# Kernel tuning notes

Hardware: AMD Instinct MI355X
Metric: run time of the kernel (lower is better)

## Reference

```python
import jax, jax.numpy as jnp
import numpy as np

B, T, C, H = 8, 2048, 1024, 64


def build_rope_cache(seq_len, dim):
    half = dim // 2
    inv_freq = 1.0 / (10000.0 ** (jnp.arange(half, dtype=jnp.float32) / half))
    t = jnp.arange(seq_len, dtype=jnp.float32)
    freqs = t[:, None] * inv_freq[None, :]          # (T, half)
    cos = jnp.repeat(jnp.cos(freqs), 2, axis=-1)    # (T, dim) interleaved
    sin = jnp.repeat(jnp.sin(freqs), 2, axis=-1)
    return cos, sin


def apply_rope(x, cos, sin):
    # x: (B, T, H); cos/sin: (T, H)
    x1 = x[..., ::2]
    x2 = x[..., 1::2]
    rot = jnp.stack([-x2, x1], axis=-1).reshape(x.shape)
    return x * cos[None] + rot * sin[None]


def setup_inputs() -> dict:
    key = jax.random.key(0)
    kx, kq, kk, kv = jax.random.split(key, 4)
    scale = 1.0 / np.sqrt(C)
    return {
        "x": jax.random.normal(kx, (B, T, C), dtype=jnp.float32),
        "Wq": jax.random.normal(kq, (C, H), dtype=jnp.float32) * scale,
        "Wk": jax.random.normal(kk, (C, H), dtype=jnp.float32) * scale,
        "Wv": jax.random.normal(kv, (C, H), dtype=jnp.float32) * scale,
    }


def reference(x, Wq, Wk, Wv):
    Bc, Tc, _ = x.shape
    head_size = Wq.shape[1]
    cos, sin = build_rope_cache(Tc, head_size)

    q = apply_rope(x @ Wq, cos, sin)   # (B, T, H)
    k = apply_rope(x @ Wk, cos, sin)   # (B, T, H)
    v = x @ Wv                          # (B, T, H)

    # full TxT masked softmax attention (matches original non-fused path)
    wei = jnp.einsum('bth,bsh->bts', q, k) * (head_size ** -0.5)  # (B, T, T)
    causal = jnp.tril(jnp.ones((Tc, Tc), dtype=bool))
    wei = jnp.where(causal[None], wei, -jnp.inf)
    wei = jax.nn.softmax(wei, axis=-1)
    # dropout p=0 (eval mode) -> identity
    return jnp.einsum('bts,bsh->bth', wei, v)
```

## Files before the change

kernel.cpp:

```cpp
#include <hip/hip_runtime.h>
#include <cmath>

#define Tn  2048
#define Cn  1024
#define Hn  64
#define BTn 16384

typedef _Float16 f16x8 __attribute__((ext_vector_type(8)));
typedef _Float16 f16x4 __attribute__((ext_vector_type(4)));
typedef _Float16 f16x2 __attribute__((ext_vector_type(2)));
typedef float    f32x4 __attribute__((ext_vector_type(4)));

__global__ __launch_bounds__(256) void prep_w_kernel(
    const float* __restrict__ Wq, const float* __restrict__ Wk,
    const float* __restrict__ Wv, _Float16* __restrict__ Wt)
{
    __shared__ float ts[64][65];
    const int blk = blockIdx.x;
    const int p   = blk >> 4;
    const int c0  = (blk & 15) * 64;
    const float* __restrict__ W = (p == 0) ? Wq : (p == 1) ? Wk : Wv;
    const int tid = threadIdx.x;
    #pragma unroll
    for (int it = 0; it < 16; it++) {
        int idx = tid + it * 256;
        int c = idx >> 6, n = idx & 63;
        ts[c][n] = W[(size_t)(c0 + c) * Hn + n];
    }
    __syncthreads();
    #pragma unroll
    for (int it = 0; it < 16; it++) {
        int idx = tid + it * 256;
        int n = idx >> 6, c = idx & 63;
        Wt[(size_t)(p * 64 + n) * Cn + c0 + c] = (_Float16)ts[c][n];
    }
}

#define XSP 1032

__global__ __launch_bounds__(256) void proj_kernel(
    const float* __restrict__ x, const _Float16* __restrict__ Wt,
    _Float16* __restrict__ qh, _Float16* __restrict__ kh, _Float16* __restrict__ vT)
{
    __shared__ _Float16 xs[32 * XSP];
    const int row0 = blockIdx.x * 32;
    const int tid  = threadIdx.x;
    const int wave = tid >> 6, lane = tid & 63;
    const int quad = lane >> 4, l15 = lane & 15;

    #pragma unroll 8
    for (int it = 0; it < 32; it++) {
        int idx = tid + it * 256;
        int r = idx >> 8, c4 = idx & 255;
        float4 xv = *(const float4*)&x[(size_t)(row0 + r) * Cn + c4 * 4];
        f16x4 hv = { (_Float16)xv.x, (_Float16)xv.y, (_Float16)xv.z, (_Float16)xv.w };
        *(f16x4*)&xs[r * XSP + c4 * 4] = hv;
    }
    __syncthreads();

    f32x4 acc[2][3] = {};
    const _Float16* __restrict__ wb = Wt + (size_t)(wave * 48 + l15) * Cn + quad * 8;

    #pragma unroll 4
    for (int kc = 0; kc < Cn; kc += 32) {
        f16x8 b0 = *(const f16x8*)&wb[kc];
        f16x8 b1 = *(const f16x8*)&wb[16 * Cn + kc];
        f16x8 b2 = *(const f16x8*)&wb[32 * Cn + kc];
        f16x8 a0 = *(const f16x8*)&xs[(     l15) * XSP + kc + quad * 8];
        f16x8 a1 = *(const f16x8*)&xs[(16 + l15) * XSP + kc + quad * 8];
        acc[0][0] = __builtin_amdgcn_mfma_f32_16x16x32_f16(a0, b0, acc[0][0], 0, 0, 0);
        acc[1][0] = __builtin_amdgcn_mfma_f32_16x16x32_f16(a1, b0, acc[1][0], 0, 0, 0);
        acc[0][1] = __builtin_amdgcn_mfma_f32_16x16x32_f16(a0, b1, acc[0][1], 0, 0, 0);
        acc[1][1] = __builtin_amdgcn_mfma_f32_16x16x32_f16(a1, b1, acc[1][1], 0, 0, 0);
        acc[0][2] = __builtin_amdgcn_mfma_f32_16x16x32_f16(a0, b2, acc[0][2], 0, 0, 0);
        acc[1][2] = __builtin_amdgcn_mfma_f32_16x16x32_f16(a1, b2, acc[1][2], 0, 0, 0);
    }

    const int bidx = row0 >> 11;
    #pragma unroll
    for (int nt = 0; nt < 3; nt++) {
        const int n = wave * 48 + nt * 16 + l15;
        const int p = n >> 6;
        const int h = n & 63;
        if (p < 2) {
            _Float16* __restrict__ outb = (p == 0) ? qh : kh;
            const float invf = __expf(-0.2878231366242557f * (float)(h >> 1));
            #pragma unroll
            for (int mt = 0; mt < 2; mt++) {
                #pragma unroll
                for (int r = 0; r < 4; r++) {
                    int   row = row0 + mt * 16 + quad * 4 + r;
                    float val = acc[mt][nt][r];
                    float partner = __shfl_xor(val, 1, 64);
                    float ang = (float)(row & (Tn - 1)) * invf;
                    float sv, cv;
                    __sincosf(ang, &sv, &cv);
                    float res = (h & 1) ? fmaf(val, cv,  partner * sv)
                                        : fmaf(val, cv, -partner * sv);
                    if (p == 0) res *= 0.125f;
                    float resn = __shfl_xor(res, 1, 64);
                    if (!(l15 & 1)) {
                        f16x2 pk = { (_Float16)res, (_Float16)resn };
                        *(f16x2*)&outb[(size_t)row * Hn + h] = pk;
                    }
                }
            }
        } else {
            #pragma unroll
            for (int mt = 0; mt < 2; mt++) {
                int t = (row0 & (Tn - 1)) + mt * 16 + quad * 4;
                f16x4 pv = { (_Float16)acc[mt][nt][0], (_Float16)acc[mt][nt][1],
                             (_Float16)acc[mt][nt][2], (_Float16)acc[mt][nt][3] };
                *(f16x4*)&vT[((size_t)bidx * Hn + h) * Tn + t] = pv;
            }
        }
    }
}

#define PSP 72

__global__ __launch_bounds__(128) void attn_kernel(
    const _Float16* __restrict__ qh, const _Float16* __restrict__ kh,
    const _Float16* __restrict__ vT, float* __restrict__ out)
{
    __shared__ _Float16 ps[2][16 * PSP];
    __shared__ float ocomb[2][16][65];
    __shared__ float mlcomb[2][2][16];

    const int blk = blockIdx.x;
    const int b   = blk & 7;
    const int j   = blk >> 3;
    const int jm  = j & 31, g = j >> 5;
    const int qt  = (g == 0) ? (127 - jm)
                  : (g == 1) ? (64 + jm)
                  : (g == 2) ? (63 - jm) : jm;
    const int t0  = qt * 16;
    const int tid = threadIdx.x;
    const int w = tid >> 6, lane = tid & 63;
    const int quad = lane >> 4, l15 = lane & 15;

    const _Float16* __restrict__ qb = qh + (size_t)b * Tn * Hn;
    const _Float16* __restrict__ kb = kh + (size_t)b * Tn * Hn;
    const _Float16* __restrict__ vb = vT + (size_t)b * Hn * Tn;

    const f16x8 aq0 = *(const f16x8*)&qb[(size_t)(t0 + l15) * Hn +      quad * 8];
    const f16x8 aq1 = *(const f16x8*)&qb[(size_t)(t0 + l15) * Hn + 32 + quad * 8];

    float m_run[4], l_run[4];
    f32x4 oacc[4] = {};
    #pragma unroll
    for (int r = 0; r < 4; r++) { m_run[r] = -1e30f; l_run[r] = 0.0f; }

    const int nst = (t0 + 16 + 63) >> 6;
    for (int jt = w; jt < nst; jt += 2) {
        const int s0 = jt * 64;

        f16x8 kf[4][2];
        #pragma unroll
        for (int nt = 0; nt < 4; nt++) {
            const _Float16* kp = &kb[(size_t)(s0 + nt * 16 + l15) * Hn + quad * 8];
            kf[nt][0] = *(const f16x8*)kp;
            kf[nt][1] = *(const f16x8*)(kp + 32);
        }
        f32x4 sacc[4];
        #pragma unroll
        for (int nt = 0; nt < 4; nt++) {
            f32x4 z = {};
            z = __builtin_amdgcn_mfma_f32_16x16x32_f16(aq0, kf[nt][0], z, 0, 0, 0);
            z = __builtin_amdgcn_mfma_f32_16x16x32_f16(aq1, kf[nt][1], z, 0, 0, 0);
            sacc[nt] = z;
        }

        f16x8 vf[2][4];
        #pragma unroll
        for (int sc = 0; sc < 2; sc++)
            #pragma unroll
            for (int ht = 0; ht < 4; ht++)
                vf[sc][ht] = *(const f16x8*)&vb[(size_t)(ht * 16 + l15) * Tn
                                                + s0 + sc * 32 + quad * 8];

        if (jt == nst - 1) {
            #pragma unroll
            for (int nt = 0; nt < 4; nt++)
                #pragma unroll
                for (int r = 0; r < 4; r++) {
                    int scol = s0 + nt * 16 + l15;
                    int trow = t0 + quad * 4 + r;
                    if (scol > trow) sacc[nt][r] = -1e30f;
                }
        }

        float pr[4][4];
        #pragma unroll
        for (int r = 0; r < 4; r++) {
            float mx = fmaxf(fmaxf(sacc[0][r], sacc[1][r]),
                             fmaxf(sacc[2][r], sacc[3][r]));
            #pragma unroll
            for (int off = 1; off < 16; off <<= 1)
                mx = fmaxf(mx, __shfl_xor(mx, off, 64));
            float mnew  = fmaxf(m_run[r], mx);
            float alpha = __expf(m_run[r] - mnew);
            m_run[r] = mnew;
            float rs = 0.0f;
            #pragma unroll
            for (int nt = 0; nt < 4; nt++) {
                float pv = __expf(sacc[nt][r] - mnew);
                pr[nt][r] = pv; rs += pv;
            }
            #pragma unroll
            for (int off = 1; off < 16; off <<= 1)
                rs += __shfl_xor(rs, off, 64);
            l_run[r] = fmaf(l_run[r], alpha, rs);
            #pragma unroll
            for (int ht = 0; ht < 4; ht++)
                oacc[ht][r] = oacc[ht][r] * alpha;
        }

        #pragma unroll
        for (int nt = 0; nt < 4; nt++)
            #pragma unroll
            for (int r = 0; r < 4; r++) {
                float pv = pr[nt][r];
                float pn = __shfl_xor(pv, 1, 64);
                if (!(l15 & 1)) {
                    f16x2 pk = { (_Float16)pv, (_Float16)pn };
                    *(f16x2*)&ps[w][(quad * 4 + r) * PSP + nt * 16 + l15] = pk;
                }
            }

        #pragma unroll
        for (int sc = 0; sc < 2; sc++) {
            f16x8 ap = *(const f16x8*)&ps[w][l15 * PSP + sc * 32 + quad * 8];
            #pragma unroll
            for (int ht = 0; ht < 4; ht++)
                oacc[ht] = __builtin_amdgcn_mfma_f32_16x16x32_f16(ap, vf[sc][ht],
                                                                  oacc[ht], 0, 0, 0);
        }
    }

    #pragma unroll
    for (int r = 0; r < 4; r++) {
        #pragma unroll
        for (int ht = 0; ht < 4; ht++)
            ocomb[w][quad * 4 + r][ht * 16 + l15] = oacc[ht][r];
        if (l15 == 0) {
            mlcomb[w][0][quad * 4 + r] = m_run[r];
            mlcomb[w][1][quad * 4 + r] = l_run[r];
        }
    }
    __syncthreads();

    #pragma unroll
    for (int rp = 0; rp < 8; rp++) {
        int row = rp * 2 + (lane >> 5);
        int h   = w * 32 + (lane & 31);
        float m0 = mlcomb[0][0][row], m1 = mlcomb[1][0][row];
        float mm = fmaxf(m0, m1);
        float a0 = __expf(m0 - mm), a1 = __expf(m1 - mm);
        float ll = mlcomb[0][1][row] * a0 + mlcomb[1][1][row] * a1;
        float ov = (ocomb[0][row][h] * a0 + ocomb[1][row][h] * a1) / ll;
        out[((size_t)b * Tn + t0 + row) * Hn + h] = ov;
    }
}

extern "C" void kernel_launch(void* const* d_in, const int* in_sizes, int n_in,
                              void* d_out, int out_size, void* d_ws, size_t ws_size,
                              hipStream_t stream) {
    const float* x  = (const float*)d_in[0];
    const float* Wq = (const float*)d_in[1];
    const float* Wk = (const float*)d_in[2];
    const float* Wv = (const float*)d_in[3];

    const size_t qkvN = (size_t)BTn * Hn;
    _Float16* qh = (_Float16*)d_ws;
    _Float16* kh = qh + qkvN;
    _Float16* vT = kh + qkvN;
    _Float16* Wt = vT + qkvN;

    prep_w_kernel<<<48, 256, 0, stream>>>(Wq, Wk, Wv, Wt);
    proj_kernel<<<BTn / 32, 256, 0, stream>>>(x, Wt, qh, kh, vT);
    attn_kernel<<<1024, 128, 0, stream>>>(qh, kh, vT, (float*)d_out);
}
```

Before: 162.7 us.

## Double waves per block in projection and attention; compute row sums via MFMA

The projection kernel moves to 8 waves per block, each owning one 16-row by 48-column tile instead of two row tiles. The attention kernel splits the key range across 4 waves instead of 2 and merges the four partial results through shared memory. It also replaces the shuffle-reduced softmax row sum with an extra MFMA against a ones vector. The aim is more parallelism per query tile and fewer cross-lane reductions, at the cost of more shared memory, a larger final merge, and B-operand reuse in the projection dropping from two row tiles to one.

```diff
diff --git a/kernel.cpp b/kernel.cpp
--- a/kernel.cpp
+++ b/kernel.cpp
@@ -38,7 +38,7 @@
 
 #define XSP 1032
 
-__global__ __launch_bounds__(256) void proj_kernel(
+__global__ __launch_bounds__(512) void proj_kernel(
     const float* __restrict__ x, const _Float16* __restrict__ Wt,
     _Float16* __restrict__ qh, _Float16* __restrict__ kh, _Float16* __restrict__ vT)
 {
@@ -47,10 +47,11 @@
     const int tid  = threadIdx.x;
     const int wave = tid >> 6, lane = tid & 63;
     const int quad = lane >> 4, l15 = lane & 15;
+    const int wr = wave >> 2, wc = wave & 3;
 
     #pragma unroll 8
-    for (int it = 0; it < 32; it++) {
-        int idx = tid + it * 256;
+    for (int it = 0; it < 16; it++) {
+        int idx = tid + it * 512;
         int r = idx >> 8, c4 = idx & 255;
         float4 xv = *(const float4*)&x[(size_t)(row0 + r) * Cn + c4 * 4];
         f16x4 hv = { (_Float16)xv.x, (_Float16)xv.y, (_Float16)xv.z, (_Float16)xv.w };
@@ -58,74 +59,64 @@
     }
     __syncthreads();
 
-    f32x4 acc[2][3] = {};
-    const _Float16* __restrict__ wb = Wt + (size_t)(wave * 48 + l15) * Cn + quad * 8;
+    f32x4 acc[3] = {};
+    const _Float16* __restrict__ wb = Wt + (size_t)(wc * 48 + l15) * Cn + quad * 8;
 
     #pragma unroll 4
     for (int kc = 0; kc < Cn; kc += 32) {
         f16x8 b0 = *(const f16x8*)&wb[kc];
         f16x8 b1 = *(const f16x8*)&wb[16 * Cn + kc];
         f16x8 b2 = *(const f16x8*)&wb[32 * Cn + kc];
-        f16x8 a0 = *(const f16x8*)&xs[(     l15) * XSP + kc + quad * 8];
-        f16x8 a1 = *(const f16x8*)&xs[(16 + l15) * XSP + kc + quad * 8];
-        acc[0][0] = __builtin_amdgcn_mfma_f32_16x16x32_f16(a0, b0, acc[0][0], 0, 0, 0);
-        acc[1][0] = __builtin_amdgcn_mfma_f32_16x16x32_f16(a1, b0, acc[1][0], 0, 0, 0);
-        acc[0][1] = __builtin_amdgcn_mfma_f32_16x16x32_f16(a0, b1, acc[0][1], 0, 0, 0);
-        acc[1][1] = __builtin_amdgcn_mfma_f32_16x16x32_f16(a1, b1, acc[1][1], 0, 0, 0);
-        acc[0][2] = __builtin_amdgcn_mfma_f32_16x16x32_f16(a0, b2, acc[0][2], 0, 0, 0);
-        acc[1][2] = __builtin_amdgcn_mfma_f32_16x16x32_f16(a1, b2, acc[1][2], 0, 0, 0);
+        f16x8 a  = *(const f16x8*)&xs[(wr * 16 + l15) * XSP + kc + quad * 8];
+        acc[0] = __builtin_amdgcn_mfma_f32_16x16x32_f16(a, b0, acc[0], 0, 0, 0);
+        acc[1] = __builtin_amdgcn_mfma_f32_16x16x32_f16(a, b1, acc[1], 0, 0, 0);
+        acc[2] = __builtin_amdgcn_mfma_f32_16x16x32_f16(a, b2, acc[2], 0, 0, 0);
     }
 
     const int bidx = row0 >> 11;
     #pragma unroll
     for (int nt = 0; nt < 3; nt++) {
-        const int n = wave * 48 + nt * 16 + l15;
+        const int n = wc * 48 + nt * 16 + l15;
         const int p = n >> 6;
         const int h = n & 63;
         if (p < 2) {
             _Float16* __restrict__ outb = (p == 0) ? qh : kh;
             const float invf = __expf(-0.2878231366242557f * (float)(h >> 1));
             #pragma unroll
-            for (int mt = 0; mt < 2; mt++) {
-                #pragma unroll
-                for (int r = 0; r < 4; r++) {
-                    int   row = row0 + mt * 16 + quad * 4 + r;
-                    float val = acc[mt][nt][r];
-                    float partner = __shfl_xor(val, 1, 64);
-                    float ang = (float)(row & (Tn - 1)) * invf;
-                    float sv, cv;
-                    __sincosf(ang, &sv, &cv);
-                    float res = (h & 1) ? fmaf(val, cv,  partner * sv)
-                                        : fmaf(val, cv, -partner * sv);
-                    if (p == 0) res *= 0.125f;
-                    float resn = __shfl_xor(res, 1, 64);
-                    if (!(l15 & 1)) {
-                        f16x2 pk = { (_Float16)res, (_Float16)resn };
-                        *(f16x2*)&outb[(size_t)row * Hn + h] = pk;
-                    }
+            for (int r = 0; r < 4; r++) {
+                int   row = row0 + wr * 16 + quad * 4 + r;
+                float val = acc[nt][r];
+                float partner = __shfl_xor(val, 1, 64);
+                float ang = (float)(row & (Tn - 1)) * invf;
+                float sv, cv;
+                __sincosf(ang, &sv, &cv);
+                float res = (h & 1) ? fmaf(val, cv,  partner * sv)
+                                    : fmaf(val, cv, -partner * sv);
+                if (p == 0) res *= 0.125f;
+                float resn = __shfl_xor(res, 1, 64);
+                if (!(l15 & 1)) {
+                    f16x2 pk = { (_Float16)res, (_Float16)resn };
+                    *(f16x2*)&outb[(size_t)row * Hn + h] = pk;
                 }
             }
         } else {
-            #pragma unroll
-            for (int mt = 0; mt < 2; mt++) {
-                int t = (row0 & (Tn - 1)) + mt * 16 + quad * 4;
-                f16x4 pv = { (_Float16)acc[mt][nt][0], (_Float16)acc[mt][nt][1],
-                             (_Float16)acc[mt][nt][2], (_Float16)acc[mt][nt][3] };
-                *(f16x4*)&vT[((size_t)bidx * Hn + h) * Tn + t] = pv;
-            }
+            int t = (row0 & (Tn - 1)) + wr * 16 + quad * 4;
+            f16x4 pv = { (_Float16)acc[nt][0], (_Float16)acc[nt][1],
+                         (_Float16)acc[nt][2], (_Float16)acc[nt][3] };
+            *(f16x4*)&vT[((size_t)bidx * Hn + h) * Tn + t] = pv;
         }
     }
 }
 
 #define PSP 72
 
-__global__ __launch_bounds__(128) void attn_kernel(
+__global__ __launch_bounds__(256) void attn_kernel(
     const _Float16* __restrict__ qh, const _Float16* __restrict__ kh,
     const _Float16* __restrict__ vT, float* __restrict__ out)
 {
-    __shared__ _Float16 ps[2][16 * PSP];
-    __shared__ float ocomb[2][16][65];
-    __shared__ float mlcomb[2][2][16];
+    __shared__ _Float16 ps[4][16 * PSP];
+    __shared__ float ocomb[4][16][68];
+    __shared__ float mlcomb[4][2][16];
 
     const int blk = blockIdx.x;
     const int b   = blk & 7;
@@ -146,13 +137,16 @@
     const f16x8 aq0 = *(const f16x8*)&qb[(size_t)(t0 + l15) * Hn +      quad * 8];
     const f16x8 aq1 = *(const f16x8*)&qb[(size_t)(t0 + l15) * Hn + 32 + quad * 8];
 
-    float m_run[4], l_run[4];
-    f32x4 oacc[4] = {};
-    #pragma unroll
-    for (int r = 0; r < 4; r++) { m_run[r] = -1e30f; l_run[r] = 0.0f; }
+    const _Float16 one1 = (_Float16)1.0f;
+    const f16x8 onesv = { one1, one1, one1, one1, one1, one1, one1, one1 };
+
+    float m_run[4];
+    f32x4 oacc[5] = {};
+    #pragma unroll
+    for (int r = 0; r < 4; r++) m_run[r] = -1e30f;
 
     const int nst = (t0 + 16 + 63) >> 6;
-    for (int jt = w; jt < nst; jt += 2) {
+    for (int jt = w; jt < nst; jt += 4) {
         const int s0 = jt * 64;
 
         f16x8 kf[4][2];
@@ -201,18 +195,11 @@
             float mnew  = fmaxf(m_run[r], mx);
             float alpha = __expf(m_run[r] - mnew);
             m_run[r] = mnew;
-            float rs = 0.0f;
-            #pragma unroll
-            for (int nt = 0; nt < 4; nt++) {
-                float pv = __expf(sacc[nt][r] - mnew);
-                pr[nt][r] = pv; rs += pv;
-            }
-            #pragma unroll
-            for (int off = 1; off < 16; off <<= 1)
-                rs += __shfl_xor(rs, off, 64);
-            l_run[r] = fmaf(l_run[r], alpha, rs);
-            #pragma unroll
-            for (int ht = 0; ht < 4; ht++)
+            #pragma unroll
+            for (int nt = 0; nt < 4; nt++)
+                pr[nt][r] = __expf(sacc[nt][r] - mnew);
+            #pragma unroll
+            for (int ht = 0; ht < 5; ht++)
                 oacc[ht][r] = oacc[ht][r] * alpha;
         }
 
@@ -235,6 +222,8 @@
             for (int ht = 0; ht < 4; ht++)
                 oacc[ht] = __builtin_amdgcn_mfma_f32_16x16x32_f16(ap, vf[sc][ht],
                                                                   oacc[ht], 0, 0, 0);
+            oacc[4] = __builtin_amdgcn_mfma_f32_16x16x32_f16(ap, onesv,
+                                                             oacc[4], 0, 0, 0);
         }
     }
 
@@ -245,21 +234,25 @@
             ocomb[w][quad * 4 + r][ht * 16 + l15] = oacc[ht][r];
         if (l15 == 0) {
             mlcomb[w][0][quad * 4 + r] = m_run[r];
-            mlcomb[w][1][quad * 4 + r] = l_run[r];
+            mlcomb[w][1][quad * 4 + r] = oacc[4][r];
         }
     }
     __syncthreads();
 
     #pragma unroll
-    for (int rp = 0; rp < 8; rp++) {
-        int row = rp * 2 + (lane >> 5);
-        int h   = w * 32 + (lane & 31);
+    for (int it = 0; it < 4; it++) {
+        int idx = tid + it * 256;
+        int row = idx >> 6, h = idx & 63;
         float m0 = mlcomb[0][0][row], m1 = mlcomb[1][0][row];
-        float mm = fmaxf(m0, m1);
+        float m2 = mlcomb[2][0][row], m3 = mlcomb[3][0][row];
+        float mm = fmaxf(fmaxf(m0, m1), fmaxf(m2, m3));
         float a0 = __expf(m0 - mm), a1 = __expf(m1 - mm);
-        float ll = mlcomb[0][1][row] * a0 + mlcomb[1][1][row] * a1;
-        float ov = (ocomb[0][row][h] * a0 + ocomb[1][row][h] * a1) / ll;
-        out[((size_t)b * Tn + t0 + row) * Hn + h] = ov;
+        float a2 = __expf(m2 - mm), a3 = __expf(m3 - mm);
+        float ll = mlcomb[0][1][row] * a0 + mlcomb[1][1][row] * a1
+                 + mlcomb[2][1][row] * a2 + mlcomb[3][1][row] * a3;
+        float ov = ocomb[0][row][h] * a0 + ocomb[1][row][h] * a1
+                 + ocomb[2][row][h] * a2 + ocomb[3][row][h] * a3;
+        out[((size_t)b * Tn + t0 + row) * Hn + h] = ov / ll;
     }
 }
 
@@ -278,6 +271,6 @@
     _Float16* Wt = vT + qkvN;
 
     prep_w_kernel<<<48, 256, 0, stream>>>(Wq, Wk, Wv, Wt);
-    proj_kernel<<<BTn / 32, 256, 0, stream>>>(x, Wt, qh, kh, vT);
-    attn_kernel<<<1024, 128, 0, stream>>>(qh, kh, vT, (float*)d_out);
-}
+    proj_kernel<<<BTn / 32, 512, 0, stream>>>(x, Wt, qh, kh, vT);
+    attn_kernel<<<1024, 256, 0, stream>>>(qh, kh, vT, (float*)d_out);
+}
```

Result: slower. 178.9 us (+9.9%).
